# Performance work log

Measured on AMD Instinct MI355X. Metric: run time of the kernel, lower is better.

## Reference

```python
import jax, jax.numpy as jnp
import numpy as np

B, L, D, H = 2, 2048, 1024, 16
HD = D // H


def setup_inputs() -> dict:
    key = jax.random.key(0)
    ks = jax.random.split(key, 8)
    x = jax.random.normal(ks[0], (B, L, D), dtype=jnp.float32)
    WQ = jax.random.normal(ks[1], (D, D), dtype=jnp.float32) * 0.02
    bQ = jnp.zeros((D,), dtype=jnp.float32)
    WK = jax.random.normal(ks[2], (D, D), dtype=jnp.float32) * 0.02
    bK = jnp.zeros((D,), dtype=jnp.float32)
    WV = jax.random.normal(ks[3], (D, D), dtype=jnp.float32) * 0.02
    bV = jnp.zeros((D,), dtype=jnp.float32)
    Wc = jax.random.normal(ks[4], (D, D), dtype=jnp.float32) * 0.02  # dense channel-mix matrix [d_out, d_in]
    return {"x": x, "WQ": WQ, "bQ": bQ, "WK": WK, "bK": bK, "WV": WV, "bV": bV, "Wc": Wc}


def reference(x, WQ, bQ, WK, bK, WV, bV, Wc):
    b, l, d = x.shape
    # --- TokenMixWeightGenerator (LOW_RANK): T = softmax(causal(Q K^T / sqrt(hd)))
    q = (x @ WQ.T + bQ).reshape(b, l, H, HD).transpose(0, 2, 1, 3)  # [B,H,L,hd]
    k = (x @ WK.T + bK).reshape(b, l, H, HD).transpose(0, 2, 1, 3)  # [B,H,L,hd]
    scores = jnp.einsum("bhid,bhjd->bhij", q, k) / jnp.sqrt(jnp.float32(HD))
    causal_mask = jnp.tril(jnp.ones((l, l), dtype=bool))  # keep j <= i
    scores = jnp.where(causal_mask, scores, -jnp.inf)
    T = jax.nn.softmax(scores, axis=-1)  # [B,H,L,L] explicit token-mix matrix
    # --- UnifiedFeaturizer (expansion=1): V reshaped per head
    v = (x @ WV.T + bV).reshape(b, l, H, HD).transpose(0, 2, 1, 3)  # [B,H,L,hd]
    # --- Y = C @ (T @ V)
    mixed = jnp.einsum("bhij,bhjd->bhid", T, v)  # [B,H,L,hd]
    mixed = mixed.transpose(0, 2, 1, 3).reshape(b, l, d)  # [B,L,D]
    y = mixed @ Wc.T  # channel mixing: output = input @ W.T
    return y
```

## Files before the change

kernel.cpp:

```cpp
#include <hip/hip_runtime.h>


typedef __bf16 bf16x8 __attribute__((ext_vector_type(8)));
typedef float f32x4 __attribute__((ext_vector_type(4)));
typedef unsigned short us4 __attribute__((ext_vector_type(4)));

#if defined(__has_builtin)
#if __has_builtin(__builtin_amdgcn_global_load_lds)
#define HAS_GLL 1
#endif
#if __has_builtin(__builtin_amdgcn_exp2f)
#define EXP2F(x) __builtin_amdgcn_exp2f(x)
#endif
#if __has_builtin(__builtin_amdgcn_mov_dpp)
#define HAS_MOVDPP 1
#endif
#endif
#ifndef HAS_GLL
#define HAS_GLL 0
#endif
#ifndef EXP2F
#define EXP2F(x) exp2f(x)
#endif

__device__ __forceinline__ float bf2f(unsigned short u) {
    union { unsigned int i; float f; } v; v.i = ((unsigned int)u) << 16; return v.f;
}
__device__ __forceinline__ unsigned short f2bf(float f) {
    union { float f; unsigned int i; } v; v.f = f;
    unsigned int r = v.i + 0x7FFFu + ((v.i >> 16) & 1u);
    return (unsigned short)(r >> 16);
}
__device__ __forceinline__ f32x4 mfma16(bf16x8 a, bf16x8 b, f32x4 c) {
    return __builtin_amdgcn_mfma_f32_16x16x32_bf16(a, b, c, 0, 0, 0);
}
__device__ __forceinline__ float clamp4(float v) {
    return fminf(fmaxf(v, -1e4f), 1e4f);
}
union U8 { unsigned short s[8]; bf16x8 v; };

__device__ __forceinline__ float swap_lane1(float x) {
#if defined(HAS_MOVDPP)
    union { float f; int i; } u; u.f = x;
    u.i = __builtin_amdgcn_mov_dpp(u.i, 0xB1, 0xF, 0xF, true);
    return u.f;
#else
    return __shfl_xor(x, 1, 64);
#endif
}

__device__ __forceinline__ unsigned int cvt_pk_bf16(float lo, float hi) {
    unsigned int r;
    asm("v_cvt_pk_bf16_f32 %0, %1, %2" : "=v"(r) : "v"(lo), "v"(hi));
    return r;
}

#if HAS_GLL
__device__ __forceinline__ void gl_lds16(const unsigned short* g, unsigned short* l) {
    __builtin_amdgcn_global_load_lds(
        (const __attribute__((address_space(1))) void*)g,
        (__attribute__((address_space(3))) void*)l, 16, 0, 0);
}
#endif


__global__ __launch_bounds__(256) void convert_all(
    const float* __restrict__ x, const float* __restrict__ WQ,
    const float* __restrict__ WK, const float* __restrict__ WV,
    const float* __restrict__ Wc,
    unsigned short* __restrict__ xbf, unsigned short* __restrict__ wbf)
{
    size_t e = ((size_t)blockIdx.x * 256 + threadIdx.x) * 8;
    const float* src; unsigned short* dst; size_t off;
    if (e < 4194304) { src = x; dst = xbf; off = e; }
    else {
        size_t j = e - 4194304; int sel = (int)(j >> 20); off = j & 1048575;
        src = (sel == 0) ? WQ : (sel == 1) ? WK : (sel == 2) ? WV : Wc;
        dst = wbf + (size_t)sel * 1048576;
    }
    f32x4 a = *(const f32x4*)(src + off);
    f32x4 b = *(const f32x4*)(src + off + 4);
    U8 u;
    u.s[0] = f2bf(a[0]); u.s[1] = f2bf(a[1]); u.s[2] = f2bf(a[2]); u.s[3] = f2bf(a[3]);
    u.s[4] = f2bf(b[0]); u.s[5] = f2bf(b[1]); u.s[6] = f2bf(b[2]); u.s[7] = f2bf(b[3]);
    *(bf16x8*)(dst + off) = u.v;
}

__global__ __launch_bounds__(256) void gemm128(
    const unsigned short* __restrict__ A, const unsigned short* __restrict__ Wbase,
    const float* __restrict__ b0, const float* __restrict__ b1, const float* __restrict__ b2,
    void* __restrict__ d0, void* __restrict__ d1, void* __restrict__ d2, int modeBase)
{
    const int z = blockIdx.z;
    const unsigned short* W = Wbase + (size_t)z * 1048576;
    const float* bias = (z == 0) ? b0 : (z == 1) ? b1 : b2;
    void* dst = (z == 0) ? d0 : (z == 1) ? d1 : d2;
    const int mode = modeBase + z;

    __shared__ __align__(16) unsigned short At[128][32];
    __shared__ __align__(16) unsigned short Bt[128][32];

    const int mb = blockIdx.y * 128, nb = blockIdx.x * 128;
    const int tid = threadIdx.x, w = tid >> 6, lane = tid & 63;
    const int wr = w >> 1, wc = w & 1;
    const int col = lane & 15, quad = lane >> 4;

    f32x4 acc[4][4];
    for (int i = 0; i < 4; ++i) for (int j = 0; j < 4; ++j) acc[i][j] = (f32x4){0.f, 0.f, 0.f, 0.f};

#if HAS_GLL
    const unsigned short* ga = A + (size_t)(mb + w * 32 + (lane >> 2)) * 1024 + (lane & 3) * 8;
    const unsigned short* gw = W + (size_t)(nb + w * 32 + (lane >> 2)) * 1024 + (lane & 3) * 8;
    unsigned short* lA0 = &At[w * 32][0];
    unsigned short* lA1 = &At[w * 32 + 16][0];
    unsigned short* lB0 = &Bt[w * 32][0];
    unsigned short* lB1 = &Bt[w * 32 + 16][0];
#else
    const int srow = w * 32 + (lane >> 1);
    const int scol = (lane & 1) * 16;
    const unsigned short* Ab = A + (size_t)(mb + srow) * 1024 + scol;
    const unsigned short* Wb = W + (size_t)(nb + srow) * 1024 + scol;
#endif

    for (int kb = 0; kb < 1024; kb += 32) {
#if HAS_GLL
        gl_lds16(ga + kb, lA0);
        gl_lds16(ga + kb + 16 * 1024, lA1);
        gl_lds16(gw + kb, lB0);
        gl_lds16(gw + kb + 16 * 1024, lB1);
#else
        *(bf16x8*)&At[srow][scol]     = *(const bf16x8*)(Ab + kb);
        *(bf16x8*)&At[srow][scol + 8] = *(const bf16x8*)(Ab + kb + 8);
        *(bf16x8*)&Bt[srow][scol]     = *(const bf16x8*)(Wb + kb);
        *(bf16x8*)&Bt[srow][scol + 8] = *(const bf16x8*)(Wb + kb + 8);
#endif
        __syncthreads();
        bf16x8 a[4], b[4];
        for (int i = 0; i < 4; ++i) a[i] = *(const bf16x8*)&At[wr * 64 + i * 16 + col][quad * 8];
        for (int j = 0; j < 4; ++j) b[j] = *(const bf16x8*)&Bt[wc * 64 + j * 16 + col][quad * 8];
        for (int i = 0; i < 4; ++i)
            for (int j = 0; j < 4; ++j)
                acc[i][j] = mfma16(a[i], b[j], acc[i][j]);
        __syncthreads();
    }

    for (int i = 0; i < 4; ++i) {
        const int mbase = mb + wr * 64 + i * 16 + quad * 4;
        const int bb = mbase >> 11, l = mbase & 2047;
        for (int j = 0; j < 4; ++j) {
            const int n = nb + wc * 64 + j * 16 + col;
            const float bv = bias ? bias[n] : 0.f;
            if (mode == 3) {
                float* o = (float*)dst;
                for (int r = 0; r < 4; ++r)
                    o[(size_t)(mbase + r) * 1024 + n] = clamp4(acc[i][j][r] + bv);
            } else if (mode == 2) {
                const int h = n >> 6, hd = n & 63;
                us4 pk;
                for (int r = 0; r < 4; ++r) pk[r] = f2bf(clamp4(acc[i][j][r] + bv));
                *(us4*)((unsigned short*)dst + (size_t)(bb * 16 + h) * 131072
                        + (size_t)hd * 2048 + l) = pk;
            } else {
                const int h = n >> 6, hd = n & 63;
                unsigned short* o = (unsigned short*)dst + (size_t)(bb * 16 + h) * 131072
                                    + (size_t)l * 64 + hd;
                for (int r = 0; r < 4; ++r)
                    o[(size_t)r * 64] = f2bf(clamp4(acc[i][j][r] + bv));
            }
        }
    }
}

__device__ __forceinline__ void attn_step(
    const unsigned short (*__restrict__ Kt)[72], const unsigned short (*__restrict__ Vt)[72],
    unsigned short (*__restrict__ Pw)[72],
    bf16x8 aq0, bf16x8 aq1, bf16x8 ones,
    f32x4* __restrict__ oacc, f32x4& lacc,
    bool diag, int col, int quad, int w, int lane)
{
    f32x4 s[4];
    for (int t = 0; t < 4; ++t) {
        bf16x8 bk0 = *(const bf16x8*)&Kt[t * 16 + col][quad * 8];
        bf16x8 bk1 = *(const bf16x8*)&Kt[t * 16 + col][32 + quad * 8];
        f32x4 z4 = (f32x4){0.f, 0.f, 0.f, 0.f};
        z4 = mfma16(aq0, bk0, z4);
        s[t] = mfma16(aq1, bk1, z4);
    }
    const int myq = w * 16 + quad * 4;
    for (int t = 0; t < 4; ++t) {
        for (int r = 0; r < 4; ++r) {
            float v = s[t][r] * 0.18033688f;
            if (diag && (t * 16 + col > myq + r)) v = -1e30f;
            v = fminf(v, 86.5f);
            s[t][r] = EXP2F(v);
        }
        for (int r = 0; r < 4; ++r) {
            float pv = s[t][r];
            float po = swap_lane1(pv);
            if (!(lane & 1))
                *(unsigned int*)&Pw[quad * 4 + r][t * 16 + col] = cvt_pk_bf16(pv, po);
        }
    }
    bf16x8 ap0 = *(const bf16x8*)&Pw[col][quad * 8];
    bf16x8 ap1 = *(const bf16x8*)&Pw[col][32 + quad * 8];
    lacc = mfma16(ap0, ones, lacc);
    lacc = mfma16(ap1, ones, lacc);
    for (int nt = 0; nt < 4; ++nt) {
        bf16x8 bv0 = *(const bf16x8*)&Vt[nt * 16 + col][quad * 8];
        bf16x8 bv1 = *(const bf16x8*)&Vt[nt * 16 + col][32 + quad * 8];
        oacc[nt] = mfma16(ap0, bv0, oacc[nt]);
        oacc[nt] = mfma16(ap1, bv1, oacc[nt]);
    }
}

__device__ __forceinline__ void attn_write(
    unsigned short* __restrict__ mixed, int gb, int h, int q0, int col, int quad,
    const f32x4* __restrict__ oacc, f32x4 lacc)
{
    f32x4 inv;
    for (int r = 0; r < 4; ++r) inv[r] = 1.f / lacc[r];
    for (int nt = 0; nt < 4; ++nt)
        for (int r = 0; r < 4; ++r) {
            int qrow = q0 + quad * 4 + r;
            mixed[(size_t)(gb * 2048 + qrow) * 1024 + h * 64 + nt * 16 + col] =
                f2bf(clamp4(oacc[nt][r] * inv[r]));
        }
}

__global__ __launch_bounds__(256) void attn_one(
    const unsigned short* __restrict__ Q, const unsigned short* __restrict__ K,
    const unsigned short* __restrict__ V, unsigned short* __restrict__ mixed)
{
    const int l = blockIdx.x;
    const int i = l & 255, kq = l >> 8;
    const int a = i & 31;
    const int qt = (kq & 1) ? (31 - a) : a;
    const int bh = (i >> 5) + 8 * kq;

    const int tid = threadIdx.x, w = tid >> 6, lane = tid & 63;
    const int col = lane & 15, quad = lane >> 4;

    __shared__ __align__(16) unsigned short Kt[64][72];
    __shared__ __align__(16) unsigned short Vt[64][72];
    __shared__ __align__(16) unsigned short Plds[4][16][72];

    const unsigned short* Qb = Q + (size_t)bh * 131072;
    const unsigned short* Kb = K + (size_t)bh * 131072;
    const unsigned short* Vb = V + (size_t)bh * 131072;

    const int q0 = qt * 64 + w * 16;
    bf16x8 aq0 = *(const bf16x8*)(Qb + (size_t)(q0 + col) * 64 + quad * 8);
    bf16x8 aq1 = *(const bf16x8*)(Qb + (size_t)(q0 + col) * 64 + 32 + quad * 8);

    U8 onesu;
    for (int j = 0; j < 8; ++j) onesu.s[j] = 0x3F80;
    const bf16x8 ones = onesu.v;

    f32x4 oacc[4];
    f32x4 lacc = (f32x4){0.f, 0.f, 0.f, 0.f};
    for (int j = 0; j < 4; ++j) oacc[j] = lacc;

    const int sr = tid >> 3, sc = (tid & 7) * 8;

    const unsigned short* kp = Kb + (size_t)sr * 64 + sc;
    const unsigned short* vp = Vb + (size_t)sr * 2048 + sc;
    bf16x8 pk0 = *(const bf16x8*)kp, pk1 = *(const bf16x8*)(kp + 32 * 64);
    bf16x8 pv0 = *(const bf16x8*)vp, pv1 = *(const bf16x8*)(vp + 32 * 2048);

    for (int kt = 0; kt <= qt; ++kt) {
        __syncthreads();
        *(bf16x8*)&Kt[sr][sc]      = pk0;
        *(bf16x8*)&Kt[sr + 32][sc] = pk1;
        *(bf16x8*)&Vt[sr][sc]      = pv0;
        *(bf16x8*)&Vt[sr + 32][sc] = pv1;
        __syncthreads();
        if (kt < qt) {
            const int kb2 = (kt + 1) * 64;
            const unsigned short* kp2 = Kb + (size_t)(kb2 + sr) * 64 + sc;
            const unsigned short* vp2 = Vb + (size_t)sr * 2048 + kb2 + sc;
            pk0 = *(const bf16x8*)kp2; pk1 = *(const bf16x8*)(kp2 + 32 * 64);
            pv0 = *(const bf16x8*)vp2; pv1 = *(const bf16x8*)(vp2 + 32 * 2048);
        }
        attn_step(Kt, Vt, Plds[w], aq0, aq1, ones, oacc, lacc, kt == qt, col, quad, w, lane);
    }

    const int gb = bh >> 4, h = bh & 15;
    attn_write(mixed, gb, h, q0, col, quad, oacc, lacc);
}


__device__ __forceinline__ bf16x8 load8(const void* base, size_t eoff, int asF32) {
    if (asF32) {
        const float* p = (const float*)base + eoff;
        f32x4 a = *(const f32x4*)p;
        f32x4 b = *(const f32x4*)(p + 4);
        U8 u;
        u.s[0]=f2bf(a[0]); u.s[1]=f2bf(a[1]); u.s[2]=f2bf(a[2]); u.s[3]=f2bf(a[3]);
        u.s[4]=f2bf(b[0]); u.s[5]=f2bf(b[1]); u.s[6]=f2bf(b[2]); u.s[7]=f2bf(b[3]);
        return u.v;
    }
    return *(const bf16x8*)((const unsigned short*)base + eoff);
}

__global__ void dtype_probe(const unsigned short* __restrict__ x, int* __restrict__ flag) {
    if (threadIdx.x == 0) {
        int c = 0;
        for (int i = 0; i < 128; ++i) {
            int e = (x[2 * i] >> 7) & 0xFF;
            if (e >= 100 && e <= 135) ++c;
        }
        *flag = (c < 64) ? 1 : 0;
    }
}

__global__ __launch_bounds__(256) void gemm_bt(
    const void* __restrict__ Ap, const void* __restrict__ Wp,
    const void* __restrict__ biasp, void* __restrict__ dout,
    unsigned short* __restrict__ wsdst, const int* __restrict__ flag,
    long aOff, long outOff, int mode, int aFlagged)
{
    const int f32 = *flag;
    __shared__ __align__(16) unsigned short At[64][32];
    __shared__ __align__(16) unsigned short Bt[64][32];
    const int mb = blockIdx.y * 64, nb = blockIdx.x * 64;
    const int tid = threadIdx.x;
    const int w = tid >> 6, lane = tid & 63;
    const int wr = w >> 1, wc = w & 1;
    const int col = lane & 15, quad = lane >> 4;
    const int srow = tid >> 2, schunk = (tid & 3) * 8;
    const int aF = aFlagged && f32;

    f32x4 acc[2][2];
    for (int i = 0; i < 2; ++i) for (int j = 0; j < 2; ++j) acc[i][j] = (f32x4){0.f,0.f,0.f,0.f};

    const size_t aBase = (size_t)aOff + (size_t)(mb + srow) * 1024 + schunk;
    const size_t wBase = (size_t)(nb + srow) * 1024 + schunk;

    for (int kb = 0; kb < 1024; kb += 32) {
        *(bf16x8*)(&At[srow][schunk]) = load8(Ap, aBase + kb, aF);
        *(bf16x8*)(&Bt[srow][schunk]) = load8(Wp, wBase + kb, f32);
        __syncthreads();
        bf16x8 a0 = *(const bf16x8*)(&At[wr * 32 + col][quad * 8]);
        bf16x8 a1 = *(const bf16x8*)(&At[wr * 32 + 16 + col][quad * 8]);
        bf16x8 b0 = *(const bf16x8*)(&Bt[wc * 32 + col][quad * 8]);
        bf16x8 b1 = *(const bf16x8*)(&Bt[wc * 32 + 16 + col][quad * 8]);
        acc[0][0] = mfma16(a0, b0, acc[0][0]);
        acc[0][1] = mfma16(a0, b1, acc[0][1]);
        acc[1][0] = mfma16(a1, b0, acc[1][0]);
        acc[1][1] = mfma16(a1, b1, acc[1][1]);
        __syncthreads();
    }

    for (int mi = 0; mi < 2; ++mi) {
        for (int ni = 0; ni < 2; ++ni) {
            int n = nb + wc * 32 + ni * 16 + col;
            float bv = 0.f;
            if (biasp) bv = f32 ? ((const float*)biasp)[n] : bf2f(((const unsigned short*)biasp)[n]);
            for (int r = 0; r < 4; ++r) {
                int m = mb + wr * 32 + mi * 16 + quad * 4 + r;
                float v = clamp4(acc[mi][ni][r] + bv);
                if (mode == 3) {
                    size_t idx = (size_t)outOff + (size_t)m * 1024 + n;
                    if (f32) ((float*)dout)[idx] = v;
                    else     ((unsigned short*)dout)[idx] = f2bf(v);
                } else {
                    int h = n >> 6, hd = n & 63;
                    size_t idx = (mode == 2)
                        ? (size_t)h * 131072 + (size_t)hd * 2048 + m
                        : (size_t)h * 131072 + (size_t)m * 64 + hd;
                    unsigned short* dstp = (mode == 0)
                        ? (unsigned short*)dout + (f32 ? 4194304 : 2097152)
                        : wsdst;
                    dstp[idx] = f2bf(v);
                }
            }
        }
    }
}

__global__ __launch_bounds__(256) void attn_kernel(
    const void* __restrict__ dout, const unsigned short* __restrict__ Kw,
    const unsigned short* __restrict__ Vw, unsigned short* __restrict__ mixed,
    const int* __restrict__ flag)
{
    const int f32 = *flag;
    const int qtile = blockIdx.x;
    const int h = blockIdx.y;
    const int w = threadIdx.x >> 6, lane = threadIdx.x & 63;
    const int col = lane & 15, quad = lane >> 4;

    __shared__ __align__(16) unsigned short Plds[4][16][64];

    const unsigned short* Qs = (const unsigned short*)dout + (f32 ? 4194304 : 2097152);
    const unsigned short* Qb = Qs + (size_t)h * 131072;
    const unsigned short* Kb = Kw + (size_t)h * 131072;
    const unsigned short* Vb = Vw + (size_t)h * 131072;

    const int q0 = qtile * 64 + w * 16;
    bf16x8 aq0 = *(const bf16x8*)(Qb + (size_t)(q0 + col) * 64 + quad * 8);
    bf16x8 aq1 = *(const bf16x8*)(Qb + (size_t)(q0 + col) * 64 + 32 + quad * 8);

    float m_run[4] = {-1e30f, -1e30f, -1e30f, -1e30f};
    float l_run[4] = {0.f, 0.f, 0.f, 0.f};
    f32x4 oacc[4];
    for (int i = 0; i < 4; ++i) oacc[i] = (f32x4){0.f, 0.f, 0.f, 0.f};

    for (int kt = 0; kt <= qtile; ++kt) {
        const int kb = kt * 64;
        f32x4 s[4];
        for (int t = 0; t < 4; ++t) {
            s[t] = (f32x4){0.f, 0.f, 0.f, 0.f};
            bf16x8 bk0 = *(const bf16x8*)(Kb + (size_t)(kb + t * 16 + col) * 64 + quad * 8);
            bf16x8 bk1 = *(const bf16x8*)(Kb + (size_t)(kb + t * 16 + col) * 64 + 32 + quad * 8);
            s[t] = mfma16(aq0, bk0, s[t]);
            s[t] = mfma16(aq1, bk1, s[t]);
        }
        for (int t = 0; t < 4; ++t)
            for (int r = 0; r < 4; ++r) {
                float v = clamp4(s[t][r] * 0.125f);
                if (kt == qtile && (t * 16 + col > w * 16 + quad * 4 + r)) v = -1e30f;
                s[t][r] = v;
            }
        float mt[4];
        for (int r = 0; r < 4; ++r)
            mt[r] = fmaxf(fmaxf(s[0][r], s[1][r]), fmaxf(s[2][r], s[3][r]));
        for (int off = 1; off < 16; off <<= 1)
            for (int r = 0; r < 4; ++r)
                mt[r] = fmaxf(mt[r], __shfl_xor(mt[r], off, 64));
        float alpha[4], rs[4], p[4][4];
        for (int r = 0; r < 4; ++r) {
            float mn = fmaxf(m_run[r], mt[r]);
            alpha[r] = __expf(m_run[r] - mn);
            m_run[r] = mn;
        }
        for (int t = 0; t < 4; ++t)
            for (int r = 0; r < 4; ++r)
                p[t][r] = __expf(s[t][r] - m_run[r]);
        for (int r = 0; r < 4; ++r)
            rs[r] = (p[0][r] + p[1][r]) + (p[2][r] + p[3][r]);
        for (int off = 1; off < 16; off <<= 1)
            for (int r = 0; r < 4; ++r)
                rs[r] += __shfl_xor(rs[r], off, 64);
        for (int r = 0; r < 4; ++r)
            l_run[r] = l_run[r] * alpha[r] + rs[r];
        for (int nt = 0; nt < 4; ++nt)
            for (int r = 0; r < 4; ++r)
                oacc[nt][r] *= alpha[r];
        for (int t = 0; t < 4; ++t)
            for (int r = 0; r < 4; ++r)
                Plds[w][quad * 4 + r][t * 16 + col] = f2bf(p[t][r]);
        __syncthreads();
        bf16x8 ap0 = *(const bf16x8*)(&Plds[w][col][quad * 8]);
        bf16x8 ap1 = *(const bf16x8*)(&Plds[w][col][32 + quad * 8]);
        for (int nt = 0; nt < 4; ++nt) {
            bf16x8 bv0 = *(const bf16x8*)(Vb + (size_t)(nt * 16 + col) * 2048 + kb + quad * 8);
            bf16x8 bv1 = *(const bf16x8*)(Vb + (size_t)(nt * 16 + col) * 2048 + kb + 32 + quad * 8);
            oacc[nt] = mfma16(ap0, bv0, oacc[nt]);
            oacc[nt] = mfma16(ap1, bv1, oacc[nt]);
        }
        __syncthreads();
    }

    float inv[4];
    for (int r = 0; r < 4; ++r) inv[r] = 1.f / l_run[r];
    for (int nt = 0; nt < 4; ++nt)
        for (int r = 0; r < 4; ++r) {
            int qrow = q0 + quad * 4 + r;
            mixed[(size_t)qrow * 1024 + h * 64 + nt * 16 + col] = f2bf(clamp4(oacc[nt][r] * inv[r]));
        }
}


extern "C" void kernel_launch(void* const* d_in, const int* in_sizes, int n_in,
                              void* d_out, int out_size, void* d_ws, size_t ws_size,
                              hipStream_t stream) {
    (void)in_sizes; (void)n_in; (void)out_size;
    const void* x  = d_in[0];
    const void* WQ = d_in[1]; const void* bQ = d_in[2];
    const void* WK = d_in[3]; const void* bK = d_in[4];
    const void* WV = d_in[5]; const void* bV = d_in[6];
    const void* Wc = d_in[7];

    if (ws_size >= (size_t)32 * 1024 * 1024) {
        unsigned short* wbf   = (unsigned short*)d_ws;
        unsigned short* Kst   = wbf + 4194304;
        unsigned short* VTst  = Kst + 4194304;
        unsigned short* mixed = VTst + 4194304;
        unsigned short* xbf   = (unsigned short*)d_out;
        unsigned short* Qst   = xbf + 4194304;

        convert_all<<<4096, 256, 0, stream>>>(
            (const float*)x, (const float*)WQ, (const float*)WK,
            (const float*)WV, (const float*)Wc, xbf, wbf);

        gemm128<<<dim3(8, 32, 3), 256, 0, stream>>>(
            xbf, wbf, (const float*)bQ, (const float*)bK, (const float*)bV,
            Qst, Kst, VTst, 0);

        attn_one<<<dim3(1024, 1), 256, 0, stream>>>(Qst, Kst, VTst, mixed);

        gemm128<<<dim3(8, 32, 1), 256, 0, stream>>>(
            mixed, wbf + 3145728, nullptr, nullptr, nullptr,
            d_out, nullptr, nullptr, 3);
    } else {
        unsigned short* wsK = (unsigned short*)d_ws;
        unsigned short* wsV = wsK + 2097152;
        unsigned short* wsM = wsV + 2097152;
        int* flag = (int*)((char*)d_ws + 12 * 1024 * 1024);

        dtype_probe<<<1, 64, 0, stream>>>((const unsigned short*)x, flag);

        dim3 gg(16, 32), gb(256);
        for (int b = 0; b < 2; ++b) {
            long xo = (long)b * 2048 * 1024;
            gemm_bt<<<gg, gb, 0, stream>>>(x, WQ, bQ, d_out, nullptr, flag, xo, 0, 0, 1);
            gemm_bt<<<gg, gb, 0, stream>>>(x, WK, bK, d_out, wsK, flag, xo, 0, 1, 1);
            gemm_bt<<<gg, gb, 0, stream>>>(x, WV, bV, d_out, wsV, flag, xo, 0, 2, 1);
            attn_kernel<<<dim3(32, 16), 256, 0, stream>>>(d_out, wsK, wsV, wsM, flag);
            gemm_bt<<<gg, gb, 0, stream>>>(wsM, Wc, nullptr, d_out, nullptr, flag,
                                           0, (long)b * 2048 * 1024, 3, 0);
        }
    }
}
```

Measured before the change: 195.6 us.

## Rewrite causal attention with 32x32 MFMA, register-resident P and 128-row query tiles

Replaces the 16x16 MFMA attention kernel with one built on 32x32x16 MFMAs. It computes S^T so that the probabilities can be packed into A-operand fragments in registers through v_permlane32_swap, which removes the LDS round trip for P and the DPP shuffles. Each block now covers 128 query rows with 4 waves, sharing K/V tiles, and the grid is halved. The row sums are accumulated with scalar adds and exchanged through a small LDS slab, replacing the ones-matrix MFMA. The risks are higher register pressure, fewer blocks available for load balancing, and waves that idle through the steps past their own diagonal.

```diff
diff --git a/kernel.cpp b/kernel.cpp
--- a/kernel.cpp
+++ b/kernel.cpp
@@ -3,6 +3,7 @@
 
 typedef __bf16 bf16x8 __attribute__((ext_vector_type(8)));
 typedef float f32x4 __attribute__((ext_vector_type(4)));
+typedef float f32x16 __attribute__((ext_vector_type(16)));
 typedef unsigned short us4 __attribute__((ext_vector_type(4)));
 
 #if defined(__has_builtin)
@@ -11,9 +12,6 @@
 #endif
 #if __has_builtin(__builtin_amdgcn_exp2f)
 #define EXP2F(x) __builtin_amdgcn_exp2f(x)
-#endif
-#if __has_builtin(__builtin_amdgcn_mov_dpp)
-#define HAS_MOVDPP 1
 #endif
 #endif
 #ifndef HAS_GLL
@@ -34,25 +32,21 @@
 __device__ __forceinline__ f32x4 mfma16(bf16x8 a, bf16x8 b, f32x4 c) {
     return __builtin_amdgcn_mfma_f32_16x16x32_bf16(a, b, c, 0, 0, 0);
 }
+__device__ __forceinline__ f32x16 mfma32(bf16x8 a, bf16x8 b, f32x16 c) {
+    return __builtin_amdgcn_mfma_f32_32x32x16_bf16(a, b, c, 0, 0, 0);
+}
 __device__ __forceinline__ float clamp4(float v) {
     return fminf(fmaxf(v, -1e4f), 1e4f);
 }
 union U8 { unsigned short s[8]; bf16x8 v; };
-
-__device__ __forceinline__ float swap_lane1(float x) {
-#if defined(HAS_MOVDPP)
-    union { float f; int i; } u; u.f = x;
-    u.i = __builtin_amdgcn_mov_dpp(u.i, 0xB1, 0xF, 0xF, true);
-    return u.f;
-#else
-    return __shfl_xor(x, 1, 64);
-#endif
-}
 
 __device__ __forceinline__ unsigned int cvt_pk_bf16(float lo, float hi) {
     unsigned int r;
     asm("v_cvt_pk_bf16_f32 %0, %1, %2" : "=v"(r) : "v"(lo), "v"(hi));
     return r;
+}
+__device__ __forceinline__ void pl32swap(unsigned int& a, unsigned int& b) {
+    asm volatile("v_permlane32_swap_b32 %0, %1" : "+v"(a), "+v"(b));
 }
 
 #if HAS_GLL
@@ -171,94 +165,107 @@
     }
 }
 
-__device__ __forceinline__ void attn_step(
+
+template<bool DIAG>
+__device__ __forceinline__ void soft_pack(
+    const f32x16& sacc, bf16x8* pa, float& lpart, int kg0, int qg)
+{
+    float p[16];
+#pragma unroll
+    for (int r = 0; r < 16; ++r) {
+        float v = sacc[r] * 0.18033688f;
+        if (DIAG) {
+            int kg = kg0 + (r & 3) + 8 * (r >> 2);
+            if (kg > qg) v = -1e30f;
+        }
+        v = fminf(v, 86.5f);
+        p[r] = EXP2F(v);
+    }
+    float t0 = (p[0] + p[1]) + (p[2] + p[3]);
+    float t1 = (p[4] + p[5]) + (p[6] + p[7]);
+    float t2 = (p[8] + p[9]) + (p[10] + p[11]);
+    float t3 = (p[12] + p[13]) + (p[14] + p[15]);
+    lpart += (t0 + t1) + (t2 + t3);
+#pragma unroll
+    for (int c = 0; c < 2; ++c) {
+        unsigned int a0 = cvt_pk_bf16(p[8*c + 0], p[8*c + 1]);
+        unsigned int b0 = cvt_pk_bf16(p[8*c + 4], p[8*c + 5]);
+        unsigned int a1 = cvt_pk_bf16(p[8*c + 2], p[8*c + 3]);
+        unsigned int b1 = cvt_pk_bf16(p[8*c + 6], p[8*c + 7]);
+        pl32swap(a0, b0);
+        pl32swap(a1, b1);
+        union PW { unsigned int w[4]; bf16x8 v; } pw;
+        pw.w[0] = a0; pw.w[1] = a1; pw.w[2] = b0; pw.w[3] = b1;
+        pa[c] = pw.v;
+    }
+}
+
+template<bool DIAG>
+__device__ __forceinline__ void attn32_step(
     const unsigned short (*__restrict__ Kt)[72], const unsigned short (*__restrict__ Vt)[72],
-    unsigned short (*__restrict__ Pw)[72],
-    bf16x8 aq0, bf16x8 aq1, bf16x8 ones,
-    f32x4* __restrict__ oacc, f32x4& lacc,
-    bool diag, int col, int quad, int w, int lane)
-{
-    f32x4 s[4];
-    for (int t = 0; t < 4; ++t) {
-        bf16x8 bk0 = *(const bf16x8*)&Kt[t * 16 + col][quad * 8];
-        bf16x8 bk1 = *(const bf16x8*)&Kt[t * 16 + col][32 + quad * 8];
-        f32x4 z4 = (f32x4){0.f, 0.f, 0.f, 0.f};
-        z4 = mfma16(aq0, bk0, z4);
-        s[t] = mfma16(aq1, bk1, z4);
-    }
-    const int myq = w * 16 + quad * 4;
-    for (int t = 0; t < 4; ++t) {
-        for (int r = 0; r < 4; ++r) {
-            float v = s[t][r] * 0.18033688f;
-            if (diag && (t * 16 + col > myq + r)) v = -1e30f;
-            v = fminf(v, 86.5f);
-            s[t][r] = EXP2F(v);
-        }
-        for (int r = 0; r < 4; ++r) {
-            float pv = s[t][r];
-            float po = swap_lane1(pv);
-            if (!(lane & 1))
-                *(unsigned int*)&Pw[quad * 4 + r][t * 16 + col] = cvt_pk_bf16(pv, po);
-        }
-    }
-    bf16x8 ap0 = *(const bf16x8*)&Pw[col][quad * 8];
-    bf16x8 ap1 = *(const bf16x8*)&Pw[col][32 + quad * 8];
-    lacc = mfma16(ap0, ones, lacc);
-    lacc = mfma16(ap1, ones, lacc);
-    for (int nt = 0; nt < 4; ++nt) {
-        bf16x8 bv0 = *(const bf16x8*)&Vt[nt * 16 + col][quad * 8];
-        bf16x8 bv1 = *(const bf16x8*)&Vt[nt * 16 + col][32 + quad * 8];
-        oacc[nt] = mfma16(ap0, bv0, oacc[nt]);
-        oacc[nt] = mfma16(ap1, bv1, oacc[nt]);
-    }
-}
-
-__device__ __forceinline__ void attn_write(
-    unsigned short* __restrict__ mixed, int gb, int h, int q0, int col, int quad,
-    const f32x4* __restrict__ oacc, f32x4 lacc)
-{
-    f32x4 inv;
-    for (int r = 0; r < 4; ++r) inv[r] = 1.f / lacc[r];
-    for (int nt = 0; nt < 4; ++nt)
-        for (int r = 0; r < 4; ++r) {
-            int qrow = q0 + quad * 4 + r;
-            mixed[(size_t)(gb * 2048 + qrow) * 1024 + h * 64 + nt * 16 + col] =
-                f2bf(clamp4(oacc[nt][r] * inv[r]));
-        }
-}
-
-__global__ __launch_bounds__(256) void attn_one(
+    const bf16x8* __restrict__ qf, f32x16* __restrict__ oacc, float& lpart,
+    int kb, int qg, int hi, int c31)
+{
+    f32x16 s0, s1;
+#pragma unroll
+    for (int r = 0; r < 16; ++r) { s0[r] = 0.f; s1[r] = 0.f; }
+#pragma unroll
+    for (int dc = 0; dc < 4; ++dc) {
+        bf16x8 kf0 = *(const bf16x8*)&Kt[c31][dc * 16 + hi * 8];
+        bf16x8 kf1 = *(const bf16x8*)&Kt[32 + c31][dc * 16 + hi * 8];
+        s0 = mfma32(kf0, qf[dc], s0);
+        s1 = mfma32(kf1, qf[dc], s1);
+    }
+    bf16x8 pa[4];
+    soft_pack<DIAG>(s0, pa,     lpart, kb + 4 * hi,      qg);
+    soft_pack<DIAG>(s1, pa + 2, lpart, kb + 32 + 4 * hi, qg);
+#pragma unroll
+    for (int b2 = 0; b2 < 2; ++b2)
+#pragma unroll
+        for (int kc = 0; kc < 4; ++kc) {
+            bf16x8 vf = *(const bf16x8*)&Vt[b2 * 32 + c31][kc * 16 + hi * 8];
+            oacc[b2] = mfma32(pa[kc], vf, oacc[b2]);
+        }
+}
+
+__global__ __launch_bounds__(256) void attn32(
     const unsigned short* __restrict__ Q, const unsigned short* __restrict__ K,
     const unsigned short* __restrict__ V, unsigned short* __restrict__ mixed)
 {
-    const int l = blockIdx.x;
-    const int i = l & 255, kq = l >> 8;
-    const int a = i & 31;
-    const int qt = (kq & 1) ? (31 - a) : a;
-    const int bh = (i >> 5) + 8 * kq;
+    const int lb = blockIdx.x;
+    const int i = lb & 255, kk = lb >> 8;
+    const int bh = i & 31, j = i >> 5;
+    const int A = kk ? (15 - j) : j;
+    const int nsteps = 2 * A + 2;
 
     const int tid = threadIdx.x, w = tid >> 6, lane = tid & 63;
-    const int col = lane & 15, quad = lane >> 4;
+    const int c31 = lane & 31, hi = lane >> 5;
 
     __shared__ __align__(16) unsigned short Kt[64][72];
     __shared__ __align__(16) unsigned short Vt[64][72];
-    __shared__ __align__(16) unsigned short Plds[4][16][72];
+    __shared__ __align__(16) float lslab[4][32];
 
     const unsigned short* Qb = Q + (size_t)bh * 131072;
     const unsigned short* Kb = K + (size_t)bh * 131072;
     const unsigned short* Vb = V + (size_t)bh * 131072;
 
-    const int q0 = qt * 64 + w * 16;
-    bf16x8 aq0 = *(const bf16x8*)(Qb + (size_t)(q0 + col) * 64 + quad * 8);
-    bf16x8 aq1 = *(const bf16x8*)(Qb + (size_t)(q0 + col) * 64 + 32 + quad * 8);
-
-    U8 onesu;
-    for (int j = 0; j < 8; ++j) onesu.s[j] = 0x3F80;
-    const bf16x8 ones = onesu.v;
-
-    f32x4 oacc[4];
-    f32x4 lacc = (f32x4){0.f, 0.f, 0.f, 0.f};
-    for (int j = 0; j < 4; ++j) oacc[j] = lacc;
+    const int q0 = A * 128 + w * 32;
+    const int qg = q0 + c31;
+    const int sstar = 2 * A + (w >> 1);
+
+    bf16x8 qf[4];
+    {
+        const unsigned short* Qr = Qb + (size_t)qg * 64 + hi * 8;
+#pragma unroll
+        for (int dc = 0; dc < 4; ++dc) qf[dc] = *(const bf16x8*)(Qr + dc * 16);
+    }
+
+    f32x16 oacc[2];
+#pragma unroll
+    for (int b2 = 0; b2 < 2; ++b2)
+#pragma unroll
+        for (int r = 0; r < 16; ++r) oacc[b2][r] = 0.f;
+    float lpart = 0.f;
 
     const int sr = tid >> 3, sc = (tid & 7) * 8;
 
@@ -267,25 +274,46 @@
     bf16x8 pk0 = *(const bf16x8*)kp, pk1 = *(const bf16x8*)(kp + 32 * 64);
     bf16x8 pv0 = *(const bf16x8*)vp, pv1 = *(const bf16x8*)(vp + 32 * 2048);
 
-    for (int kt = 0; kt <= qt; ++kt) {
+    for (int s = 0; s < nsteps; ++s) {
         __syncthreads();
         *(bf16x8*)&Kt[sr][sc]      = pk0;
         *(bf16x8*)&Kt[sr + 32][sc] = pk1;
         *(bf16x8*)&Vt[sr][sc]      = pv0;
         *(bf16x8*)&Vt[sr + 32][sc] = pv1;
         __syncthreads();
-        if (kt < qt) {
-            const int kb2 = (kt + 1) * 64;
+        if (s + 1 < nsteps) {
+            const int kb2 = (s + 1) * 64;
             const unsigned short* kp2 = Kb + (size_t)(kb2 + sr) * 64 + sc;
             const unsigned short* vp2 = Vb + (size_t)sr * 2048 + kb2 + sc;
             pk0 = *(const bf16x8*)kp2; pk1 = *(const bf16x8*)(kp2 + 32 * 64);
             pv0 = *(const bf16x8*)vp2; pv1 = *(const bf16x8*)(vp2 + 32 * 2048);
         }
-        attn_step(Kt, Vt, Plds[w], aq0, aq1, ones, oacc, lacc, kt == qt, col, quad, w, lane);
-    }
+        if (s < sstar)
+            attn32_step<false>(Kt, Vt, qf, oacc, lpart, s * 64, qg, hi, c31);
+        else if (s == sstar)
+            attn32_step<true >(Kt, Vt, qf, oacc, lpart, s * 64, qg, hi, c31);
+    }
+
+    float ltot = lpart + __shfl_xor(lpart, 32, 64);
+    if (lane < 32) lslab[w][lane] = ltot;
+    f32x4 lv[4];
+#pragma unroll
+    for (int m = 0; m < 4; ++m) lv[m] = *(const f32x4*)&lslab[w][4 * hi + 8 * m];
+    f32x4 iv[4];
+#pragma unroll
+    for (int m = 0; m < 4; ++m)
+#pragma unroll
+        for (int r = 0; r < 4; ++r) iv[m][r] = 1.f / lv[m][r];
 
     const int gb = bh >> 4, h = bh & 15;
-    attn_write(mixed, gb, h, q0, col, quad, oacc, lacc);
+#pragma unroll
+    for (int b2 = 0; b2 < 2; ++b2)
+#pragma unroll
+        for (int r = 0; r < 16; ++r) {
+            const int qrow = q0 + 4 * hi + (r & 3) + 8 * (r >> 2);
+            const float val = clamp4(oacc[b2][r] * iv[r >> 2][r & 3]);
+            mixed[(size_t)(gb * 2048 + qrow) * 1024 + h * 64 + b2 * 32 + c31] = f2bf(val);
+        }
 }
 
 
@@ -497,7 +525,7 @@
             xbf, wbf, (const float*)bQ, (const float*)bK, (const float*)bV,
             Qst, Kst, VTst, 0);
 
-        attn_one<<<dim3(1024, 1), 256, 0, stream>>>(Qst, Kst, VTst, mixed);
+        attn32<<<dim3(512, 1), 256, 0, stream>>>(Qst, Kst, VTst, mixed);
 
         gemm128<<<dim3(8, 32, 1), 256, 0, stream>>>(
             mixed, wbf + 3145728, nullptr, nullptr, nullptr,
```

Result: faster. 186.4 us (-4.7%).
